# Kernel tuning notes

Measured on AMD Instinct MI355X. Metric: run time of the kernel, lower is better.

The kernel has to match this reference:

```python
import jax, jax.numpy as jnp
import numpy as np

N, E, D_IN, D_OUT, SIZE = 50000, 800000, 128, 128, 4
NEG_SLOPE = 0.01  # torch leaky_relu default


def setup_inputs() -> dict:
    key = jax.random.key(0)
    k1, k2, k3, k4, k5 = jax.random.split(key, 5)
    x = jax.random.normal(k1, (N, D_IN), dtype=jnp.float32)
    edge_index = jax.random.randint(k2, (2, E), 0, N, dtype=jnp.int32)
    s = 1.0 / np.sqrt(D_IN)
    W_l = jax.random.uniform(k3, (SIZE, D_IN, D_OUT), jnp.float32, -s, s)
    W_r = jax.random.uniform(k4, (SIZE, D_IN, D_OUT), jnp.float32, -s, s)
    b = jax.random.uniform(k5, (SIZE, D_OUT), jnp.float32, -s, s)
    return {"x": x, "edge_index": edge_index, "W_l": W_l, "W_r": W_r, "b": b}


def reference(x, edge_index, W_l, W_r, b):
    src, dst = edge_index[0], edge_index[1]
    # mean aggregation of source features into destination nodes (shared by all heads)
    agg = jax.ops.segment_sum(x[src], dst, num_segments=N)          # [N, D_IN]
    cnt = jax.ops.segment_sum(jnp.ones((E, 1), x.dtype), dst, num_segments=N)
    mean_nbr = agg / jnp.maximum(cnt, 1.0)
    # per-head SAGEConv: lin_l(mean_nbr) + lin_r(x) + b, batched over heads
    h = (jnp.einsum('nd,sdo->nso', mean_nbr, W_l)
         + jnp.einsum('nd,sdo->nso', x, W_r)
         + b[None, :, :])                                           # [N, SIZE, D_OUT]
    h = jnp.where(h > 0, h, NEG_SLOPE * h)                          # leaky_relu
    return h.reshape(N, SIZE * D_OUT)                               # concat over heads
```

## Files before the change

### kernel.cpp

```cpp
#include <hip/hip_runtime.h>

#define NN    50000
#define NE    800000
#define DIN   128
#define NH    4
#define NEG   0.01f
#define NROWS 50048
#define NBKT  1024
#define BD    49
#define NBLK  391
#define EPB   2048
#define NXBF  3128
#define EBUF  2048
#define QS    21.166666667f
#define QSI   0.047244094f

typedef __attribute__((ext_vector_type(8))) short short8v;
typedef __attribute__((ext_vector_type(8))) ushort ushort8v;
typedef __attribute__((ext_vector_type(4))) float float4v;

__device__ __forceinline__ ushort f2bf(float f) {
    union { float f; unsigned u; } c; c.f = f;
    unsigned u = c.u;
    return (ushort)((u + 0x7FFFu + ((u >> 16) & 1u)) >> 16);
}

__device__ __forceinline__ void async16(void* lds, const void* g) {
    __builtin_amdgcn_global_load_lds(
        (const __attribute__((address_space(1))) unsigned*)g,
        (__attribute__((address_space(3))) unsigned*)lds, 16, 0, 0);
}

__global__ __launch_bounds__(256) void k_prep(const float* __restrict__ x,
                                              const float* __restrict__ Wl,
                                              const float* __restrict__ Wr,
                                              ushort* __restrict__ A,
                                              unsigned* __restrict__ xq,
                                              ushort* __restrict__ Bt,
                                              int* __restrict__ cursor) {
    const int bid = blockIdx.x, t = threadIdx.x;
    if (bid < NXBF) {
        const int tid = bid * 256 + t;
        const int n = tid >> 4, seg = tid & 15;
        ushort8v o;
        unsigned w0 = 0, w1 = 0;
        if (n < NN) {
            const float4* xp = (const float4*)(x + (size_t)n * DIN + seg * 8);
            float4 v0 = xp[0], v1 = xp[1];
            float v[8] = {v0.x, v0.y, v0.z, v0.w, v1.x, v1.y, v1.z, v1.w};
            unsigned q[8];
            #pragma unroll
            for (int i = 0; i < 8; ++i) {
                o[i] = f2bf(v[i]);
                int qi = (int)rintf(fminf(fmaxf(v[i] * QS, -127.f), 127.f));
                q[i] = (unsigned)qi & 0xFFu;
            }
            w0 = q[0] | (q[1] << 8) | (q[2] << 16) | (q[3] << 24);
            w1 = q[4] | (q[5] << 8) | (q[6] << 16) | (q[7] << 24);
        } else {
            #pragma unroll
            for (int i = 0; i < 8; ++i) o[i] = 0;
        }
        *(ushort8v*)(A + (size_t)n * 256 + 128 + seg * 8) = o;
        *(uint2*)(xq + (size_t)n * 32 + seg * 2) = make_uint2(w0, w1);
    } else if (bid < NXBF + 64) {
        const int tid = (bid - NXBF) * 256 + t;
        const int j = tid >> 5, kc = tid & 31;
        const int s = j >> 7, col = j & 127;
        short8v o;
        #pragma unroll
        for (int i = 0; i < 8; ++i) {
            int k = kc * 8 + i;
            float w = (k < 128) ? Wl[((size_t)s * DIN + k) * 128 + col]
                                : Wr[((size_t)s * DIN + (k - 128)) * 128 + col];
            o[i] = (short)f2bf(w);
        }
        *(short8v*)(Bt + (size_t)j * 256 + kc * 8) = o;
    } else {
        for (int i = t; i < NBKT; i += 256) cursor[i] = i * EBUF;
    }
}

__global__ __launch_bounds__(256) void k_pscat(const int* __restrict__ ei,
                                               int* __restrict__ cursor,
                                               unsigned* __restrict__ ebkt) {
    __shared__ int h[NBKT];
    __shared__ int lcur[NBKT];
    const int t = threadIdx.x, blk = blockIdx.x;
    for (int i = t; i < NBKT; i += 256) h[i] = 0;
    __syncthreads();
    const int base = blk * EPB;
    int dsts[8];
    #pragma unroll
    for (int i = 0; i < 8; ++i) {
        const int e = base + i * 256 + t;
        if (e < NE) {
            dsts[i] = ei[NE + e];
            atomicAdd(&h[dsts[i] / BD], 1);
        }
    }
    __syncthreads();
    for (int i = t; i < NBKT; i += 256) {
        const int c = h[i];
        lcur[i] = c ? atomicAdd(&cursor[i], c) : 0;
    }
    __syncthreads();
    #pragma unroll
    for (int i = 0; i < 8; ++i) {
        const int e = base + i * 256 + t;
        if (e < NE) {
            const int src = ei[e];
            const int dst = dsts[i];
            const int b = dst / BD;
            const int r = atomicAdd(&lcur[b], 1);
            ebkt[r] = ((unsigned)dst << 16) | (unsigned)src;
        }
    }
}

#define ACC1(w, k)                              \
    {                                           \
        acc[(k) + 0] += (int)((w) << 24) >> 24; \
        acc[(k) + 1] += (int)((w) << 16) >> 24; \
        acc[(k) + 2] += (int)((w) << 8) >> 24;  \
        acc[(k) + 3] += (int)(w) >> 24;         \
    }
#define ACC4(v) { ACC1((v).x, 0) ACC1((v).y, 4) ACC1((v).z, 8) ACC1((v).w, 12) }

__global__ __launch_bounds__(256) void k_bg(const unsigned* __restrict__ ebkt,
                                            const int* __restrict__ cursor,
                                            const unsigned* __restrict__ xq,
                                            ushort* __restrict__ A) {
    __shared__ unsigned ebuf[EBUF];
    __shared__ ushort lsrc[EBUF];
    __shared__ int lcnt[BD], loff[BD], lcur[BD];
    const int t = threadIdx.x, b = blockIdx.x;
    const int d0 = b * BD;
    const int s0 = b * EBUF;
    int cnt = cursor[b] - s0;
    if (cnt > EBUF) cnt = EBUF;
    if (cnt < 0) cnt = 0;
    if (t < BD) { lcnt[t] = 0; lcur[t] = 0; }
    __syncthreads();
    for (int e = t; e < cnt; e += 256) {
        const unsigned u = ebkt[s0 + e];
        ebuf[e] = u;
        atomicAdd(&lcnt[(int)(u >> 16) - d0], 1);
    }
    __syncthreads();
    if (t == 0) {
        int run = 0;
        #pragma unroll
        for (int i = 0; i < BD; ++i) { loff[i] = run; run += lcnt[i]; }
    }
    __syncthreads();
    for (int e = t; e < cnt; e += 256) {
        const unsigned u = ebuf[e];
        const int dl = (int)(u >> 16) - d0;
        const int r = atomicAdd(&lcur[dl], 1);
        lsrc[loff[dl] + r] = (ushort)(u & 0xFFFFu);
    }
    __syncthreads();

    const int gl = t & 7;
    for (int dl = t >> 3; dl < BD; dl += 32) {
        const int n = d0 + dl;
        if (n >= NROWS) break;
        const int deg = lcnt[dl], base = loff[dl];
        int acc[16];
        #pragma unroll
        for (int i = 0; i < 16; ++i) acc[i] = 0;
        int j = 0;
        for (; j + 4 <= deg; j += 4) {
            const int e0 = lsrc[base + j], e1 = lsrc[base + j + 1];
            const int e2 = lsrc[base + j + 2], e3 = lsrc[base + j + 3];
            uint4 v0 = *(const uint4*)(xq + (size_t)e0 * 32 + gl * 4);
            uint4 v1 = *(const uint4*)(xq + (size_t)e1 * 32 + gl * 4);
            uint4 v2 = *(const uint4*)(xq + (size_t)e2 * 32 + gl * 4);
            uint4 v3 = *(const uint4*)(xq + (size_t)e3 * 32 + gl * 4);
            ACC4(v0) ACC4(v1) ACC4(v2) ACC4(v3)
        }
        for (; j < deg; ++j) {
            const int e0 = lsrc[base + j];
            uint4 v = *(const uint4*)(xq + (size_t)e0 * 32 + gl * 4);
            ACC4(v)
        }
        const float invq = (n < NN) ? QSI / (float)(deg > 1 ? deg : 1) : 0.f;
        ushort8v o0, o1;
        #pragma unroll
        for (int i = 0; i < 8; ++i) o0[i] = f2bf((float)acc[i] * invq);
        #pragma unroll
        for (int i = 0; i < 8; ++i) o1[i] = f2bf((float)acc[8 + i] * invq);
        ushort* dst = A + (size_t)n * 256 + gl * 16;
        *(ushort8v*)dst = o0;
        *(ushort8v*)(dst + 8) = o1;
    }
}

__global__ __launch_bounds__(256, 2) void k_mm(const ushort* __restrict__ A,
                                               const ushort* __restrict__ Bt,
                                               const float* __restrict__ bias,
                                               float* __restrict__ out)
{
    __shared__ ushort sA[64 * 256];
    const int t = threadIdx.x;
    const int wid = t >> 6, l = t & 63;
    const int node0 = blockIdx.x * 64;

    {
        const int chunk = l & 31;
        #pragma unroll
        for (int inst = 0; inst < 8; ++inst) {
            const int row = wid * 16 + inst * 2 + (l >> 5);
            const ushort* src = A + (size_t)(node0 + row) * 256
                                  + ((chunk ^ (row & 7)) * 8);
            ushort* dst = &sA[(wid * 16 + inst * 2) * 256];
            async16(dst, src);
        }
    }
    __syncthreads();

    const int lr = l & 15;
    const int lk = l >> 4;
    const ushort* bt = Bt + (size_t)wid * 128 * 256;

    float4v acc[4][8];
    #pragma unroll
    for (int m = 0; m < 4; ++m)
        #pragma unroll
        for (int n = 0; n < 8; ++n)
            acc[m][n] = (float4v){0.f, 0.f, 0.f, 0.f};

    #pragma unroll
    for (int kt = 0; kt < 8; ++kt) {
        short8v af[4];
        #pragma unroll
        for (int m = 0; m < 4; ++m) {
            const int row = m * 16 + lr;
            const int gch = kt * 4 + lk;
            af[m] = *(const short8v*)&sA[row * 256 + ((gch ^ (row & 7)) * 8)];
        }
        short8v bf[8];
        #pragma unroll
        for (int n = 0; n < 8; ++n)
            bf[n] = *(const short8v*)&bt[(size_t)(n * 16 + lr) * 256 + kt * 32 + lk * 8];
        #pragma unroll
        for (int n = 0; n < 8; ++n)
            #pragma unroll
            for (int m = 0; m < 4; ++m)
                acc[m][n] = __builtin_amdgcn_mfma_f32_16x16x32_bf16(af[m], bf[n], acc[m][n], 0, 0, 0);
    }

    float bcol[8];
    #pragma unroll
    for (int n = 0; n < 8; ++n) bcol[n] = bias[wid * 128 + n * 16 + lr];

    #pragma unroll
    for (int m = 0; m < 4; ++m) {
        #pragma unroll
        for (int r = 0; r < 4; ++r) {
            const int node = node0 + m * 16 + lk * 4 + r;
            if (node < NN) {
                float* op = out + (size_t)node * (NH * DIN) + wid * 128 + lr;
                #pragma unroll
                for (int n = 0; n < 8; ++n) {
                    float h = acc[m][n][r] + bcol[n];
                    op[n * 16] = h > 0.f ? h : NEG * h;
                }
            }
        }
    }
}

extern "C" void kernel_launch(void* const* d_in, const int* in_sizes, int n_in,
                              void* d_out, int out_size, void* d_ws, size_t ws_size,
                              hipStream_t stream) {
    const float* x  = (const float*)d_in[0];
    const int*   ei = (const int*)d_in[1];
    const float* Wl = (const float*)d_in[2];
    const float* Wr = (const float*)d_in[3];
    const float* b  = (const float*)d_in[4];
    float* out = (float*)d_out;

    ushort*   A      = (ushort*)d_ws;
    ushort*   Bt     = A + (size_t)NROWS * 256;
    unsigned* xq     = (unsigned*)(Bt + 512 * 256);
    unsigned* ebkt   = xq + (size_t)NROWS * 32;
    int*      cursor = (int*)(ebkt + (size_t)NBKT * EBUF);

    k_prep <<<NXBF + 64 + 1, 256, 0, stream>>>(x, Wl, Wr, A, xq, Bt, cursor);
    k_pscat<<<NBLK, 256, 0, stream>>>(ei, cursor, ebkt);
    k_bg   <<<NBKT, 256, 0, stream>>>(ebkt, cursor, xq, A);
    k_mm   <<<NROWS / 64, 256, 0, stream>>>(A, Bt, b, out);
}
```

Before: 102.7 us.

## Merge edge bucketing into the prep kernel and unroll gather loop by eight

The edge-scatter work from k_pscat moves into the same launch as the x quantization and weight transpose, with the scatter blocks placed first. Cursor initialization goes into its own tiny kernel. This lets the independent bucketing and conversion work overlap in one grid and saves a dependent launch. The gather loop in k_bg also gains an 8-wide unroll so more loads are in flight. In exchange there is one extra small launch, and the prep-path blocks now also reserve the 8KB of shared memory the scatter path uses, which may lower their occupancy.

```diff
diff --git a/kernel.cpp b/kernel.cpp
--- a/kernel.cpp
+++ b/kernel.cpp
@@ -31,16 +31,55 @@
         (__attribute__((address_space(3))) unsigned*)lds, 16, 0, 0);
 }
 
-__global__ __launch_bounds__(256) void k_prep(const float* __restrict__ x,
+__global__ __launch_bounds__(256) void k_init(int* __restrict__ cursor) {
+    for (int i = threadIdx.x; i < NBKT; i += 256) cursor[i] = i * EBUF;
+}
+
+__global__ __launch_bounds__(256) void k_work(const float* __restrict__ x,
                                               const float* __restrict__ Wl,
                                               const float* __restrict__ Wr,
+                                              const int* __restrict__ ei,
                                               ushort* __restrict__ A,
                                               unsigned* __restrict__ xq,
                                               ushort* __restrict__ Bt,
-                                              int* __restrict__ cursor) {
+                                              int* __restrict__ cursor,
+                                              unsigned* __restrict__ ebkt) {
+    __shared__ int h[NBKT];
+    __shared__ int lcur[NBKT];
     const int bid = blockIdx.x, t = threadIdx.x;
-    if (bid < NXBF) {
-        const int tid = bid * 256 + t;
+    if (bid < NBLK) {
+        const int blk = bid;
+        for (int i = t; i < NBKT; i += 256) h[i] = 0;
+        __syncthreads();
+        const int base = blk * EPB;
+        int dsts[8];
+        #pragma unroll
+        for (int i = 0; i < 8; ++i) {
+            const int e = base + i * 256 + t;
+            if (e < NE) {
+                dsts[i] = ei[NE + e];
+                atomicAdd(&h[dsts[i] / BD], 1);
+            }
+        }
+        __syncthreads();
+        for (int i = t; i < NBKT; i += 256) {
+            const int c = h[i];
+            lcur[i] = c ? atomicAdd(&cursor[i], c) : 0;
+        }
+        __syncthreads();
+        #pragma unroll
+        for (int i = 0; i < 8; ++i) {
+            const int e = base + i * 256 + t;
+            if (e < NE) {
+                const int src = ei[e];
+                const int dst = dsts[i];
+                const int b = dst / BD;
+                const int r = atomicAdd(&lcur[b], 1);
+                ebkt[r] = ((unsigned)dst << 16) | (unsigned)src;
+            }
+        }
+    } else if (bid < NBLK + NXBF) {
+        const int tid = (bid - NBLK) * 256 + t;
         const int n = tid >> 4, seg = tid & 15;
         ushort8v o;
         unsigned w0 = 0, w1 = 0;
@@ -63,8 +102,8 @@
         }
         *(ushort8v*)(A + (size_t)n * 256 + 128 + seg * 8) = o;
         *(uint2*)(xq + (size_t)n * 32 + seg * 2) = make_uint2(w0, w1);
-    } else if (bid < NXBF + 64) {
-        const int tid = (bid - NXBF) * 256 + t;
+    } else {
+        const int tid = (bid - NBLK - NXBF) * 256 + t;
         const int j = tid >> 5, kc = tid & 31;
         const int s = j >> 7, col = j & 127;
         short8v o;
@@ -76,45 +115,6 @@
             o[i] = (short)f2bf(w);
         }
         *(short8v*)(Bt + (size_t)j * 256 + kc * 8) = o;
-    } else {
-        for (int i = t; i < NBKT; i += 256) cursor[i] = i * EBUF;
-    }
-}
-
-__global__ __launch_bounds__(256) void k_pscat(const int* __restrict__ ei,
-                                               int* __restrict__ cursor,
-                                               unsigned* __restrict__ ebkt) {
-    __shared__ int h[NBKT];
-    __shared__ int lcur[NBKT];
-    const int t = threadIdx.x, blk = blockIdx.x;
-    for (int i = t; i < NBKT; i += 256) h[i] = 0;
-    __syncthreads();
-    const int base = blk * EPB;
-    int dsts[8];
-    #pragma unroll
-    for (int i = 0; i < 8; ++i) {
-        const int e = base + i * 256 + t;
-        if (e < NE) {
-            dsts[i] = ei[NE + e];
-            atomicAdd(&h[dsts[i] / BD], 1);
-        }
-    }
-    __syncthreads();
-    for (int i = t; i < NBKT; i += 256) {
-        const int c = h[i];
-        lcur[i] = c ? atomicAdd(&cursor[i], c) : 0;
-    }
-    __syncthreads();
-    #pragma unroll
-    for (int i = 0; i < 8; ++i) {
-        const int e = base + i * 256 + t;
-        if (e < NE) {
-            const int src = ei[e];
-            const int dst = dsts[i];
-            const int b = dst / BD;
-            const int r = atomicAdd(&lcur[b], 1);
-            ebkt[r] = ((unsigned)dst << 16) | (unsigned)src;
-        }
     }
 }
 
@@ -171,18 +171,27 @@
         #pragma unroll
         for (int i = 0; i < 16; ++i) acc[i] = 0;
         int j = 0;
+        for (; j + 8 <= deg; j += 8) {
+            uint4 v0 = *(const uint4*)(xq + (size_t)lsrc[base + j] * 32 + gl * 4);
+            uint4 v1 = *(const uint4*)(xq + (size_t)lsrc[base + j + 1] * 32 + gl * 4);
+            uint4 v2 = *(const uint4*)(xq + (size_t)lsrc[base + j + 2] * 32 + gl * 4);
+            uint4 v3 = *(const uint4*)(xq + (size_t)lsrc[base + j + 3] * 32 + gl * 4);
+            uint4 v4 = *(const uint4*)(xq + (size_t)lsrc[base + j + 4] * 32 + gl * 4);
+            uint4 v5 = *(const uint4*)(xq + (size_t)lsrc[base + j + 5] * 32 + gl * 4);
+            uint4 v6 = *(const uint4*)(xq + (size_t)lsrc[base + j + 6] * 32 + gl * 4);
+            uint4 v7 = *(const uint4*)(xq + (size_t)lsrc[base + j + 7] * 32 + gl * 4);
+            ACC4(v0) ACC4(v1) ACC4(v2) ACC4(v3)
+            ACC4(v4) ACC4(v5) ACC4(v6) ACC4(v7)
+        }
         for (; j + 4 <= deg; j += 4) {
-            const int e0 = lsrc[base + j], e1 = lsrc[base + j + 1];
-            const int e2 = lsrc[base + j + 2], e3 = lsrc[base + j + 3];
-            uint4 v0 = *(const uint4*)(xq + (size_t)e0 * 32 + gl * 4);
-            uint4 v1 = *(const uint4*)(xq + (size_t)e1 * 32 + gl * 4);
-            uint4 v2 = *(const uint4*)(xq + (size_t)e2 * 32 + gl * 4);
-            uint4 v3 = *(const uint4*)(xq + (size_t)e3 * 32 + gl * 4);
+            uint4 v0 = *(const uint4*)(xq + (size_t)lsrc[base + j] * 32 + gl * 4);
+            uint4 v1 = *(const uint4*)(xq + (size_t)lsrc[base + j + 1] * 32 + gl * 4);
+            uint4 v2 = *(const uint4*)(xq + (size_t)lsrc[base + j + 2] * 32 + gl * 4);
+            uint4 v3 = *(const uint4*)(xq + (size_t)lsrc[base + j + 3] * 32 + gl * 4);
             ACC4(v0) ACC4(v1) ACC4(v2) ACC4(v3)
         }
         for (; j < deg; ++j) {
-            const int e0 = lsrc[base + j];
-            uint4 v = *(const uint4*)(xq + (size_t)e0 * 32 + gl * 4);
+            uint4 v = *(const uint4*)(xq + (size_t)lsrc[base + j] * 32 + gl * 4);
             ACC4(v)
         }
         const float invq = (n < NN) ? QSI / (float)(deg > 1 ? deg : 1) : 0.f;
@@ -288,8 +297,8 @@
     unsigned* ebkt   = xq + (size_t)NROWS * 32;
     int*      cursor = (int*)(ebkt + (size_t)NBKT * EBUF);
 
-    k_prep <<<NXBF + 64 + 1, 256, 0, stream>>>(x, Wl, Wr, A, xq, Bt, cursor);
-    k_pscat<<<NBLK, 256, 0, stream>>>(ei, cursor, ebkt);
-    k_bg   <<<NBKT, 256, 0, stream>>>(ebkt, cursor, xq, A);
-    k_mm   <<<NROWS / 64, 256, 0, stream>>>(A, Bt, b, out);
-}
+    k_init<<<1, 256, 0, stream>>>(cursor);
+    k_work<<<NBLK + NXBF + 64, 256, 0, stream>>>(x, Wl, Wr, ei, A, xq, Bt, cursor, ebkt);
+    k_bg  <<<NBKT, 256, 0, stream>>>(ebkt, cursor, xq, A);
+    k_mm  <<<NROWS / 64, 256, 0, stream>>>(A, Bt, b, out);
+}
```

Result: faster. 100.5 us (-2.1%).
